# Kernel optimization log

Hardware: AMD Instinct MI355X
Metric: run time of the kernel (lower is better)

## Reference

```python
import jax, jax.numpy as jnp
import numpy as np

N, F_IN, H, P, R = 50000, 384, 128, 128, 16
E = 500000


def _lin_params(key, fan_in, fan_out):
    k1, k2 = jax.random.split(key)
    s = 1.0 / np.sqrt(fan_in)
    W = jax.random.uniform(k1, (fan_in, fan_out), jnp.float32, -s, s)
    b = jax.random.uniform(k2, (fan_out,), jnp.float32, -s, s)
    return W, b


def setup_inputs() -> dict:
    key = jax.random.key(0)
    ks = jax.random.split(key, 16)
    x = jax.random.normal(ks[0], (N, F_IN), jnp.float32)
    edge_index = jax.random.randint(ks[1], (2, E), 0, N, jnp.int64)
    W_gcn1, b_gcn1 = _lin_params(ks[2], F_IN, H)
    W_ti, b_ti = _lin_params(ks[3], F_IN, F_IN)      # CrossFusion.text_info (384 -> dim=384)
    W_gi, b_gi = _lin_params(ks[4], H, F_IN)          # CrossFusion.graph_info (128 -> 384)
    W_v, b_v = _lin_params(ks[5], F_IN, F_IN)         # CrossFusion.value
    Wl1, bl1 = _lin_params(ks[6], F_IN, F_IN // 2)    # left_generator hidden
    Wl2, bl2 = _lin_params(ks[7], F_IN // 2, P * R)
    Wr1, br1 = _lin_params(ks[8], F_IN, F_IN // 2)    # right_generator hidden
    Wr2, br2 = _lin_params(ks[9], F_IN // 2, R * F_IN)
    W_gcn2, b_gcn2 = _lin_params(ks[10], P, H)        # fusion_gcn (128 -> 128)
    W_gp, b_gp = _lin_params(ks[11], P, P)            # graph_proj
    return dict(x=x, edge_index=edge_index, W_gcn1=W_gcn1, b_gcn1=b_gcn1,
                W_ti=W_ti, b_ti=b_ti, W_gi=W_gi, b_gi=b_gi, W_v=W_v, b_v=b_v,
                Wl1=Wl1, bl1=bl1, Wl2=Wl2, bl2=bl2, Wr1=Wr1, br1=br1, Wr2=Wr2, br2=br2,
                W_gcn2=W_gcn2, b_gcn2=b_gcn2, W_gp=W_gp, b_gp=b_gp)


def _gcn(x, W, b, src, dst, n):
    # PyG GCNConv: self-loops + symmetric degree normalization, aggregate at dst.
    xw = x @ W
    loop = jnp.arange(n, dtype=src.dtype)
    s = jnp.concatenate([src, loop])
    d = jnp.concatenate([dst, loop])
    deg = jax.ops.segment_sum(jnp.ones_like(d, dtype=xw.dtype), d, num_segments=n)
    dinv = jnp.where(deg > 0, jax.lax.rsqrt(deg), 0.0)
    norm = dinv[s] * dinv[d]                           # [E+N]
    out = jax.ops.segment_sum(norm[:, None] * xw[s], d, num_segments=n)
    return out + b


def _cross_fusion(text_feat, graph_feat, row, col, W_ti, b_ti, W_gi, b_gi, W_v, b_v):
    n, dim = text_feat.shape[0], W_ti.shape[1]
    t_info = text_feat @ W_ti + b_ti                   # [N, dim]
    g_info = graph_feat @ W_gi + b_gi                  # [N, dim]
    v = text_feat @ W_v + b_v                          # [N, dim]
    scores = jnp.sum(t_info[row] * g_info[col], axis=-1) / np.sqrt(dim)   # [E]
    m = jax.ops.segment_max(scores, row, num_segments=n)                  # scatter_softmax
    e = jnp.exp(scores - m[row])
    denom = jax.ops.segment_sum(e, row, num_segments=n)
    attn = e / denom[row]
    out = jax.ops.segment_sum(attn[:, None] * v[col], row, num_segments=n)
    return out + text_feat


def _forward(x, edge_index, W_gcn1, b_gcn1, W_ti, b_ti, W_gi, b_gi, W_v, b_v,
             Wl1, bl1, Wl2, bl2, Wr1, br1, Wr2, br2, W_gcn2, b_gcn2, W_gp, b_gp):
    src, dst = edge_index[0], edge_index[1]
    n = x.shape[0]
    g_emb = _gcn(x, W_gcn1, b_gcn1, src, dst, n)
    x_fused = _cross_fusion(x, g_emb, src, dst, W_ti, b_ti, W_gi, b_gi, W_v, b_v)
    # N > 40000 -> low-rank chunked projection (chunking is pure batching; vectorize)
    left = (jax.nn.relu(x_fused @ Wl1 + bl1) @ Wl2 + bl2).reshape(n, P, R)
    right = (jax.nn.relu(x_fused @ Wr1 + br1) @ Wr2 + br2).reshape(n, R, F_IN)
    temp = jnp.einsum('nrf,nf->nr', right, x)
    p_t = jnp.einsum('npr,nr->np', left, temp)         # [N, P]
    g2 = _gcn(p_t, W_gcn2, b_gcn2, src, dst, n)        # dropout is identity in eval
    p_g = g2 @ W_gp + b_gp
    p_t = p_t / jnp.maximum(jnp.linalg.norm(p_t, axis=-1, keepdims=True), 1e-12)
    p_g = p_g / jnp.maximum(jnp.linalg.norm(p_g, axis=-1, keepdims=True), 1e-12)
    alignment = jnp.sum(p_t * p_g, axis=1)
    return alignment, p_t, p_g, g2


def reference(x, edge_index, W_gcn1, b_gcn1, W_ti, b_ti, W_gi, b_gi, W_v, b_v,
              Wl1, bl1, Wl2, bl2, Wr1, br1, Wr2, br2, W_gcn2, b_gcn2, W_gp, b_gp):
    return _forward(x, edge_index, W_gcn1, b_gcn1, W_ti, b_ti, W_gi, b_gi, W_v, b_v,
                    Wl1, bl1, Wl2, bl2, Wr1, br1, Wr2, br2, W_gcn2, b_gcn2, W_gp, b_gp)
```

## Files before the change

### kernel.cpp

```cpp
#include <hip/hip_runtime.h>

typedef unsigned int u32;
typedef unsigned short u16;
typedef short s16x8 __attribute__((ext_vector_type(8)));
typedef u16 u16x8 __attribute__((ext_vector_type(8)));
typedef float f32x4 __attribute__((ext_vector_type(4)));

#define FIN 384
#define HD  128
#define PD  128
#define RD  16

#define GLOAD16(g, l)                                                          \
  __builtin_amdgcn_global_load_lds(                                            \
      (const __attribute__((address_space(1))) void*)(g),                      \
      (__attribute__((address_space(3))) void*)(l), 16, 0, 0)

__device__ __forceinline__ u16 f2bf(float f) {
  u32 u = __float_as_uint(f);
  u32 r = (u + 0x7fffu + ((u >> 16) & 1u)) >> 16;
  return (u16)r;
}
__device__ __forceinline__ float bf2f(u16 h) {
  return __uint_as_float(((u32)h) << 16);
}

__device__ __forceinline__ int xcd_wgid() {
  int nwg = gridDim.x, orig = blockIdx.x;
  int q = nwg >> 3, r = nwg & 7, xcd = orig & 7, idx = orig >> 3;
  return (xcd < r ? xcd * (q + 1) : r * (q + 1) + (xcd - r) * q) + idx;
}

struct CvtEnt { const float* s; u16* d; int K, N, mode, blk0; };
struct CvtDesc { CvtEnt e[12]; int n; };

__global__ void cvt_all_k(CvtDesc dsc) {
  int b = blockIdx.x;
  int ei = 0;
  while (ei + 1 < dsc.n && dsc.e[ei + 1].blk0 <= b) ++ei;
  CvtEnt E = dsc.e[ei];
  int i = (b - E.blk0) * 256 + (int)threadIdx.x;
  int tot = E.K * E.N;
  if (i >= tot) return;
  float v;
  if (E.mode == 0) {
    int c = i / E.K, k = i - c * E.K;
    v = E.s[(size_t)k * E.N + c];
  } else if (E.mode == 1) {
    v = E.s[i];
  } else {
    int q = i / 384, f = i - q * 384;
    v = E.s[(size_t)(q >> 4) * 6144 + (q & 15) * 384 + f];
  }
  E.d[i] = f2bf(v);
}

__global__ void hist_k(const int* __restrict__ src, const int* __restrict__ dst,
                       u32* __restrict__ cnt, int n, int E) {
  int i = blockIdx.x * 256 + threadIdx.x;
  if (i < E) {
    atomicAdd(&cnt[src[i]], 1u);
    atomicAdd(&cnt[n + dst[i]], 1u);
  }
}

__global__ __launch_bounds__(1024)
void scanA_k(const u32* __restrict__ cnt, u32* __restrict__ off,
             u32* __restrict__ bsum, int n2) {
  __shared__ u32 sh[1024];
  int i = blockIdx.x * 1024 + (int)threadIdx.x;
  u32 v = (i < n2) ? cnt[i] : 0u;
  sh[threadIdx.x] = v;
  __syncthreads();
  for (int s = 1; s < 1024; s <<= 1) {
    u32 t = (threadIdx.x >= (u32)s) ? sh[threadIdx.x - s] : 0u;
    __syncthreads();
    sh[threadIdx.x] += t;
    __syncthreads();
  }
  if (i < n2) off[i] = sh[threadIdx.x] - v;
  if (threadIdx.x == 1023) bsum[blockIdx.x] = sh[1023];
}

__global__ void scanB_k(u32* __restrict__ bsum, int nb) {
  int l = threadIdx.x;
  u32 carry = 0u;
  for (int base = 0; base < nb; base += 64) {
    u32 v = (base + l < nb) ? bsum[base + l] : 0u;
    for (int s = 1; s < 64; s <<= 1) {
      u32 t = __shfl_up(v, s);
      if (l >= s) v += t;
    }
    if (base + l < nb) bsum[base + l] = v + carry;
    carry += __shfl(v, 63);
  }
}

__global__ __launch_bounds__(1024)
void scanC_k(u32* __restrict__ off, u32* __restrict__ cur,
             const u32* __restrict__ bsum, int n2) {
  int b = blockIdx.x;
  int i = b * 1024 + (int)threadIdx.x;
  if (i >= n2) return;
  u32 add = (b > 0) ? bsum[b - 1] : 0u;
  u32 o = off[i] + add;
  off[i] = o;
  cur[i] = o;
}

__global__ void fill_k(const int* __restrict__ src, const int* __restrict__ dst,
                       u32* __restrict__ cur, u32* __restrict__ adj, int n, int E) {
  int i = blockIdx.x * 256 + threadIdx.x;
  if (i >= E) return;
  int s = src[i], d = dst[i];
  u32 ps = atomicAdd(&cur[s], 1u);
  adj[ps] = (u32)d;
  u32 pd = atomicAdd(&cur[n + d], 1u);
  adj[pd] = (u32)s;
}

__global__ void dinv_k(const u32* __restrict__ cd, float* __restrict__ dinv, int n) {
  int i = blockIdx.x * 256 + threadIdx.x;
  if (i < n) dinv[i] = 1.0f / sqrtf((float)(cd[i] + 1u));
}

template <int WF32, int WBF>
__global__ void gcn_agg_k(const u16* __restrict__ xw, const float* __restrict__ dinv,
                          const u32* __restrict__ off, const u32* __restrict__ cnt,
                          const u32* __restrict__ nbr, const float* __restrict__ bias,
                          float* __restrict__ outf, u16* __restrict__ outb, int n) {
  int node = (blockIdx.x * blockDim.x + threadIdx.x) >> 6;
  int lane = threadIdx.x & 63;
  if (node >= n) return;
  float di = dinv[node];
  ushort2 v = ((const ushort2*)(xw + (size_t)node * HD))[lane];
  float ax = di * di * bf2f(v.x), ay = di * di * bf2f(v.y);
  u32 i = off[node], end = i + cnt[node];
  for (; i + 2 <= end; i += 2) {
    int s0 = (int)nbr[i], s1 = (int)nbr[i + 1];
    float w0 = di * dinv[s0], w1 = di * dinv[s1];
    ushort2 u0 = ((const ushort2*)(xw + (size_t)s0 * HD))[lane];
    ushort2 u1 = ((const ushort2*)(xw + (size_t)s1 * HD))[lane];
    ax = fmaf(w0, bf2f(u0.x), ax);
    ay = fmaf(w0, bf2f(u0.y), ay);
    ax = fmaf(w1, bf2f(u1.x), ax);
    ay = fmaf(w1, bf2f(u1.y), ay);
  }
  if (i < end) {
    int s0 = (int)nbr[i];
    float w0 = di * dinv[s0];
    ushort2 u0 = ((const ushort2*)(xw + (size_t)s0 * HD))[lane];
    ax = fmaf(w0, bf2f(u0.x), ax);
    ay = fmaf(w0, bf2f(u0.y), ay);
  }
  float2 b = ((const float2*)bias)[lane];
  ax += b.x; ay += b.y;
  if (WF32) ((float2*)(outf + (size_t)node * HD))[lane] = make_float2(ax, ay);
  if (WBF) {
    ushort2 ob; ob.x = f2bf(ax); ob.y = f2bf(ay);
    ((ushort2*)(outb + (size_t)node * HD))[lane] = ob;
  }
}

__global__ void attn_fused_k(const u32* __restrict__ off, const u32* __restrict__ cnt,
                             const u32* __restrict__ adj,
                             const u16* __restrict__ ti, int TS,
                             const u16* __restrict__ gi, int GS,
                             const u16* __restrict__ vmat, int VS,
                             const u16* __restrict__ xb,
                             float* __restrict__ scores,
                             u16* __restrict__ xf, int n) {
  int node = (blockIdx.x * blockDim.x + threadIdx.x) >> 6;
  int lane = threadIdx.x & 63;
  if (node >= n) return;
  u32 o = off[node], c = cnt[node];
  u32 end = o + c;
  float acc[6] = {0.f, 0.f, 0.f, 0.f, 0.f, 0.f};
  if (c > 0) {
    const u16* tp = ti + (size_t)node * TS;
    float tf[6];
#pragma unroll
    for (int q = 0; q < 3; ++q) {
      ushort2 tv = *(const ushort2*)(tp + q * 128 + lane * 2);
      tf[q * 2] = bf2f(tv.x);
      tf[q * 2 + 1] = bf2f(tv.y);
    }
    const float sc = 0.05103103630798288f;
    float mx = -1e30f;
    u32 i = o;
    for (; i + 2 <= end; i += 2) {
      int d0 = (int)adj[i], d1 = (int)adj[i + 1];
      const u16* g0 = gi + (size_t)d0 * GS;
      const u16* g1 = gi + (size_t)d1 * GS;
      float dot0 = 0.f, dot1 = 0.f;
#pragma unroll
      for (int q = 0; q < 3; ++q) {
        ushort2 a = *(const ushort2*)(g0 + q * 128 + lane * 2);
        ushort2 b = *(const ushort2*)(g1 + q * 128 + lane * 2);
        dot0 = fmaf(tf[q * 2], bf2f(a.x), dot0);
        dot0 = fmaf(tf[q * 2 + 1], bf2f(a.y), dot0);
        dot1 = fmaf(tf[q * 2], bf2f(b.x), dot1);
        dot1 = fmaf(tf[q * 2 + 1], bf2f(b.y), dot1);
      }
#pragma unroll
      for (int s2 = 32; s2 >= 1; s2 >>= 1) {
        dot0 += __shfl_xor(dot0, s2);
        dot1 += __shfl_xor(dot1, s2);
      }
      dot0 *= sc; dot1 *= sc;
      if (lane == 0) { scores[i] = dot0; scores[i + 1] = dot1; }
      mx = fmaxf(mx, fmaxf(dot0, dot1));
    }
    if (i < end) {
      int d0 = (int)adj[i];
      const u16* g0 = gi + (size_t)d0 * GS;
      float dot0 = 0.f;
#pragma unroll
      for (int q = 0; q < 3; ++q) {
        ushort2 a = *(const ushort2*)(g0 + q * 128 + lane * 2);
        dot0 = fmaf(tf[q * 2], bf2f(a.x), dot0);
        dot0 = fmaf(tf[q * 2 + 1], bf2f(a.y), dot0);
      }
#pragma unroll
      for (int s2 = 32; s2 >= 1; s2 >>= 1) dot0 += __shfl_xor(dot0, s2);
      dot0 *= sc;
      if (lane == 0) scores[i] = dot0;
      mx = fmaxf(mx, dot0);
    }
    float den = 0.f;
    for (u32 k = o + lane; k < end; k += 64) den += expf(scores[k] - mx);
#pragma unroll
    for (int s2 = 32; s2 >= 1; s2 >>= 1) den += __shfl_xor(den, s2);
    float invden = 1.0f / den;
    i = o;
    for (; i + 2 <= end; i += 2) {
      int d0 = (int)adj[i], d1 = (int)adj[i + 1];
      float w0 = expf(scores[i] - mx) * invden;
      float w1 = expf(scores[i + 1] - mx) * invden;
      const u16* v0 = vmat + (size_t)d0 * VS;
      const u16* v1 = vmat + (size_t)d1 * VS;
#pragma unroll
      for (int q = 0; q < 3; ++q) {
        ushort2 a = *(const ushort2*)(v0 + q * 128 + lane * 2);
        ushort2 b = *(const ushort2*)(v1 + q * 128 + lane * 2);
        acc[q * 2]     = fmaf(w0, bf2f(a.x), acc[q * 2]);
        acc[q * 2 + 1] = fmaf(w0, bf2f(a.y), acc[q * 2 + 1]);
        acc[q * 2]     = fmaf(w1, bf2f(b.x), acc[q * 2]);
        acc[q * 2 + 1] = fmaf(w1, bf2f(b.y), acc[q * 2 + 1]);
      }
    }
    if (i < end) {
      int d0 = (int)adj[i];
      float w0 = expf(scores[i] - mx) * invden;
      const u16* v0 = vmat + (size_t)d0 * VS;
#pragma unroll
      for (int q = 0; q < 3; ++q) {
        ushort2 a = *(const ushort2*)(v0 + q * 128 + lane * 2);
        acc[q * 2]     = fmaf(w0, bf2f(a.x), acc[q * 2]);
        acc[q * 2 + 1] = fmaf(w0, bf2f(a.y), acc[q * 2 + 1]);
      }
    }
  }
  const u16* xp = xb + (size_t)node * FIN;
  u16* op = xf + (size_t)node * FIN;
#pragma unroll
  for (int q = 0; q < 3; ++q) {
    ushort2 xv = *(const ushort2*)(xp + q * 128 + lane * 2);
    ushort2 ov;
    ov.x = f2bf(acc[q * 2] + bf2f(xv.x));
    ov.y = f2bf(acc[q * 2 + 1] + bf2f(xv.y));
    *(ushort2*)(op + q * 128 + lane * 2) = ov;
  }
}

template <int EPI, int OUTBF>
__global__ __launch_bounds__(256)
void mgemm_k(const u16* __restrict__ Abf, int As, const u16* __restrict__ WT,
             const float* __restrict__ bias, const float* __restrict__ bias_b, int bsplit,
             void* __restrict__ Cp, u16* __restrict__ Cbf2,
             float* __restrict__ tmp, int M, int K, int Nc, int ncx) {
  __shared__ u16 Albuf[2][128 * 32];
  __shared__ u16 Blbuf[2][128 * 32];
  const int t = threadIdx.x;
  const int lane = t & 63;
  const int wave = t >> 6;
  const int wr = wave >> 1, wc = wave & 1;
  const int wgid = xcd_wgid();
  const int ctile = wgid % ncx;
  const int row0 = (wgid / ncx) * 128;
  const int col0 = ctile * 128;
  const int sr = t >> 2;
  const int sk = (t & 3) * 8;
  const int nt = K >> 5;

  f32x4 acc[4][4] = {};

  auto stage = [&](int buf, int k0) {
#pragma unroll
    for (int h = 0; h < 2; ++h) {
      int ar = row0 + h * 64 + sr;
      if (ar >= M) ar = M - 1;
      GLOAD16(Abf + (size_t)ar * As + k0 + sk, &Albuf[buf][h * 2048 + wave * 512]);
    }
#pragma unroll
    for (int h = 0; h < 2; ++h) {
      int bc = col0 + h * 64 + sr;
      if (bc >= Nc) bc = Nc - 1;
      GLOAD16(WT + (size_t)bc * K + k0 + sk, &Blbuf[buf][h * 2048 + wave * 512]);
    }
  };

  stage(0, 0);
  int buf = 0;
  for (int tk = 0; tk < nt; ++tk) {
    __syncthreads();
    if (tk + 1 < nt) stage(buf ^ 1, (tk + 1) << 5);
    const u16* Al = Albuf[buf];
    const u16* Bl = Blbuf[buf];
    s16x8 a[4], b[4];
#pragma unroll
    for (int m = 0; m < 4; ++m)
      a[m] = *(const s16x8*)(Al + (wr * 64 + m * 16 + (lane & 15)) * 32 + (lane >> 4) * 8);
#pragma unroll
    for (int j = 0; j < 4; ++j)
      b[j] = *(const s16x8*)(Bl + (wc * 64 + j * 16 + (lane & 15)) * 32 + (lane >> 4) * 8);
#pragma unroll
    for (int m = 0; m < 4; ++m)
#pragma unroll
      for (int j = 0; j < 4; ++j)
        acc[m][j] = __builtin_amdgcn_mfma_f32_16x16x32_bf16(a[m], b[j], acc[m][j], 0, 0, 0);
    buf ^= 1;
  }

  if constexpr (EPI <= 2) {
#pragma unroll
    for (int m = 0; m < 4; ++m) {
      int rbase = row0 + wr * 64 + m * 16 + (lane >> 4) * 4;
#pragma unroll
      for (int j = 0; j < 4; ++j) {
        int col = col0 + wc * 64 + j * 16 + (lane & 15);
        if (col >= Nc) continue;
        float bv = 0.f;
        if (EPI >= 1) bv = (col < bsplit) ? bias[col] : bias_b[col - bsplit];
#pragma unroll
        for (int r = 0; r < 4; ++r) {
          int row = rbase + r;
          if (row >= M) continue;
          float v = acc[m][j][r] + bv;
          if (EPI == 2) v = fmaxf(v, 0.f);
          if (OUTBF) ((u16*)Cp)[(size_t)row * Nc + col] = f2bf(v);
          else       ((float*)Cp)[(size_t)row * Nc + col] = v;
        }
      }
    }
  } else if constexpr (EPI == 6) {
#pragma unroll
    for (int m = 0; m < 4; ++m) {
      int rbase = row0 + wr * 64 + m * 16 + (lane >> 4) * 4;
#pragma unroll
      for (int j = 0; j < 4; ++j) {
        int col = col0 + wc * 64 + j * 16 + (lane & 15);
        if (col < 2 * FIN) {
          float bv = (col < bsplit) ? bias[col] : bias_b[col - bsplit];
#pragma unroll
          for (int r = 0; r < 4; ++r) {
            int row = rbase + r;
            if (row >= M) continue;
            ((u16*)Cp)[(size_t)row * (2 * FIN) + col] = f2bf(acc[m][j][r] + bv);
          }
        } else {
          int c2 = col - 2 * FIN;
#pragma unroll
          for (int r = 0; r < 4; ++r) {
            int row = rbase + r;
            if (row >= M) continue;
            Cbf2[(size_t)row * HD + c2] = f2bf(acc[m][j][r]);
          }
        }
      }
    }
  } else {
    float* slice = (float*)Cp + (size_t)ctile * M * 8;
#pragma unroll
    for (int m = 0; m < 4; ++m) {
#pragma unroll
      for (int r = 0; r < 4; ++r) {
        int row = row0 + wr * 64 + m * 16 + (lane >> 4) * 4 + r;
        float tv = (row < M) ? tmp[(size_t)row * RD + (lane & 15)] : 0.f;
#pragma unroll
        for (int j = 0; j < 4; ++j) {
          float s = (acc[m][j][r] + bias[col0 + wc * 64 + j * 16 + (lane & 15)]) * tv;
          s += __shfl_xor(s, 1); s += __shfl_xor(s, 2);
          s += __shfl_xor(s, 4); s += __shfl_xor(s, 8);
          if ((lane & 15) == 0 && row < M)
            slice[(size_t)row * 8 + wc * 4 + j] = s;
        }
      }
    }
  }
}

__global__ void ptgather_k(const float* __restrict__ ptP, float* __restrict__ pt,
                           u16* __restrict__ ptb, int n) {
  int g = blockIdx.x * 256 + threadIdx.x;
  if (g >= n * 16) return;
  int row = g >> 4, ct = g & 15;
  const float* sp = ptP + ((size_t)ct * n + (size_t)row) * 8;
  float4 a = ((const float4*)sp)[0];
  float4 b = ((const float4*)sp)[1];
  float* dp = pt + (size_t)row * PD + ct * 8;
  ((float4*)dp)[0] = a;
  ((float4*)dp)[1] = b;
  ushort4 oa, ob;
  oa.x = f2bf(a.x); oa.y = f2bf(a.y); oa.z = f2bf(a.z); oa.w = f2bf(a.w);
  ob.x = f2bf(b.x); ob.y = f2bf(b.y); ob.z = f2bf(b.z); ob.w = f2bf(b.w);
  u16* db = ptb + (size_t)row * PD + ct * 8;
  ((ushort4*)db)[0] = oa;
  ((ushort4*)db)[1] = ob;
}

#define VM6  asm volatile("s_waitcnt vmcnt(6)" ::: "memory")
#define VM0  asm volatile("s_waitcnt vmcnt(0)" ::: "memory")
#define VMNOP
#define BARR asm volatile("s_barrier" ::: "memory")

__global__ __launch_bounds__(512)
void ygemm8_k(const u16* __restrict__ X, const u16* __restrict__ QT,
              const u16* __restrict__ Ar, float* __restrict__ tmpP, int M) {
  __shared__ u16 Al[2][16384];
  __shared__ u16 Bl[2][16384];
  const int t = threadIdx.x;
  const int lane = t & 63;
  const int wave = t >> 6;
  const int wr = wave >> 2;
  const int wcn = wave & 3;
  const int wgid = xcd_wgid();
  const int ctile = wgid % 12;
  const int row0 = (wgid / 12) * 256;
  const int col0 = ctile * 256;

  const int srow = t >> 3;
  const int sgk  = (((t & 7) ^ (srow & 7)) << 3);
  const int sdst = t * 8;

  const int pc0 = (((lane >> 4)) ^ (lane & 7)) << 3;
  const int pc1 = ((((lane >> 4) + 4)) ^ (lane & 7)) << 3;
  const int arow = (wr * 128 + (lane & 15)) << 6;
  const int brow = (wcn * 64 + (lane & 15)) << 6;

  f32x4 acc[8][4] = {};
  s16x8 a[4][2], b[4][2];

#define STGA8(bf, h, kt) do {                                                  \
    int r0_ = row0 + (h) * 128 + srow;                                         \
    int r1_ = r0_ + 64;                                                        \
    if (r0_ >= M) r0_ = M - 1;                                                 \
    if (r1_ >= M) r1_ = M - 1;                                                 \
    GLOAD16(X + (size_t)r0_ * 384 + (kt) * 64 + sgk, &Al[bf][(h) * 8192 + sdst]);        \
    GLOAD16(X + (size_t)r1_ * 384 + (kt) * 64 + sgk, &Al[bf][(h) * 8192 + 4096 + sdst]); \
  } while (0)

#define STGB8(bf, h, kt) do {                                                  \
    int c0_ = col0 + (h) * 128 + srow;                                         \
    GLOAD16(QT + (size_t)c0_ * 384 + (kt) * 64 + sgk, &Bl[bf][(h) * 8192 + sdst]);       \
    GLOAD16(QT + (size_t)(c0_ + 64) * 384 + (kt) * 64 + sgk,                   \
            &Bl[bf][(h) * 8192 + 4096 + sdst]);                                \
  } while (0)

#define LDA8(bf, mh) do {                                                      \
    _Pragma("unroll") for (int m2_ = 0; m2_ < 4; ++m2_) {                      \
      const u16* p_ = &Al[bf][arow + ((mh) * 4 + m2_) * 1024];                 \
      a[m2_][0] = *(const s16x8*)(p_ + pc0);                                   \
      a[m2_][1] = *(const s16x8*)(p_ + pc1);                                   \
    }                                                                          \
  } while (0)

#define LDB8(bf, jh) do {                                                      \
    _Pragma("unroll") for (int j2_ = 0; j2_ < 2; ++j2_) {                      \
      const u16* p_ = &Bl[bf][brow + ((jh) * 2 + j2_) * 1024];                 \
      b[(jh) * 2 + j2_][0] = *(const s16x8*)(p_ + pc0);                        \
      b[(jh) * 2 + j2_][1] = *(const s16x8*)(p_ + pc1);                        \
    }                                                                          \
  } while (0)

#define MQ8(mh, jh) do {                                                       \
    __builtin_amdgcn_s_setprio(1);                                             \
    _Pragma("unroll") for (int m2_ = 0; m2_ < 4; ++m2_)                        \
      _Pragma("unroll") for (int j2_ = 0; j2_ < 2; ++j2_)                      \
        _Pragma("unroll") for (int ks_ = 0; ks_ < 2; ++ks_)                    \
          acc[(mh) * 4 + m2_][(jh) * 2 + j2_] =                                \
              __builtin_amdgcn_mfma_f32_16x16x32_bf16(                         \
                  a[m2_][ks_], b[(jh) * 2 + j2_][ks_],                         \
                  acc[(mh) * 4 + m2_][(jh) * 2 + j2_], 0, 0, 0);               \
    __builtin_amdgcn_s_setprio(0);                                             \
  } while (0)

  STGA8(0, 0, 0); STGA8(0, 1, 0); STGB8(0, 0, 0); STGB8(0, 1, 0);
  STGA8(1, 0, 1); STGB8(1, 0, 1); STGB8(1, 1, 1);
  VM6; BARR;

#define ITER8(i, VMP3, VMP7, DOSTG)                                                          \
   LDA8(0,0); LDB8(0,0); STGA8(1,1,2*(i)+1);                   BARR; MQ8(0,0); BARR;  \
   LDB8(0,1);                                                  BARR; MQ8(0,1); BARR;  \
   LDA8(0,1); if (DOSTG) STGB8(0,0,2*(i)+2);                   BARR; MQ8(1,0); BARR;  \
   if (DOSTG) { STGB8(0,1,2*(i)+2); STGA8(0,0,2*(i)+2); } VMP3; BARR; MQ8(1,1); BARR; \
   LDA8(1,0); LDB8(1,0); if (DOSTG) STGA8(0,1,2*(i)+2);        BARR; MQ8(0,0); BARR;  \
   LDB8(1,1);                                                  BARR; MQ8(0,1); BARR;  \
   LDA8(1,1); if (DOSTG) STGB8(1,0,2*(i)+3);                   BARR; MQ8(1,0); BARR;  \
   if (DOSTG) { STGB8(1,1,2*(i)+3); STGA8(1,0,2*(i)+3); } VMP7; BARR; MQ8(1,1); BARR;

  ITER8(0, VM6, VM6, 1)
  ITER8(1, VM6, VM6, 1)
  ITER8(2, VM0, VMNOP, 0)

  const int h0 = (col0 >> 4) + wcn * 4;
  float s[8][4];
#pragma unroll
  for (int m = 0; m < 8; ++m) {
#pragma unroll
    for (int rr = 0; rr < 4; ++rr) {
      int row = row0 + wr * 128 + m * 16 + (lane >> 4) * 4 + rr;
      int rc = row < M ? row : M - 1;
      ushort4 arv = *(const ushort4*)(Ar + (size_t)rc * 384 + h0);
      s[m][rr] = bf2f(arv.x) * acc[m][0][rr] + bf2f(arv.y) * acc[m][1][rr] +
                 bf2f(arv.z) * acc[m][2][rr] + bf2f(arv.w) * acc[m][3][rr];
    }
  }

  __syncthreads();
  float* redA = (float*)&Al[0][0];
  float* redB = redA + 4096;
  const int r16 = lane & 15;
  const int rlb = wr * 128 + (lane >> 4) * 4;
  if (wcn & 1) {
    float* red = (wcn == 1) ? redA : redB;
#pragma unroll
    for (int m = 0; m < 8; ++m)
#pragma unroll
      for (int rr = 0; rr < 4; ++rr)
        red[(rlb + m * 16 + rr) * 16 + r16] = s[m][rr];
  }
  __syncthreads();
  if (!(wcn & 1)) {
    float* red = (wcn == 0) ? redA : redB;
#pragma unroll
    for (int m = 0; m < 8; ++m)
#pragma unroll
      for (int rr = 0; rr < 4; ++rr)
        s[m][rr] += red[(rlb + m * 16 + rr) * 16 + r16];
  }
  __syncthreads();
  if (wcn == 2) {
#pragma unroll
    for (int m = 0; m < 8; ++m)
#pragma unroll
      for (int rr = 0; rr < 4; ++rr)
        redA[(rlb + m * 16 + rr) * 16 + r16] = s[m][rr];
  }
  __syncthreads();
  if (wcn == 0) {
    float* slice = tmpP + (size_t)ctile * M * RD;
#pragma unroll
    for (int m = 0; m < 8; ++m)
#pragma unroll
      for (int rr = 0; rr < 4; ++rr) {
        int row = row0 + rlb + m * 16 + rr;
        if (row < M)
          slice[(size_t)row * RD + r16] =
              s[m][rr] + redA[(rlb + m * 16 + rr) * 16 + r16];
      }
  }
#undef STGA8
#undef STGB8
#undef LDA8
#undef LDB8
#undef MQ8
#undef ITER8
}

__global__ void combine_k(const float* __restrict__ tmpP, float* __restrict__ temp,
                          size_t sl, int tot4) {
  int i = blockIdx.x * 256 + threadIdx.x;
  if (i >= tot4) return;
  float4 s = ((const float4*)(tmpP + 12 * sl))[i];
#pragma unroll
  for (int c = 0; c < 12; ++c) {
    float4 p = ((const float4*)(tmpP + (size_t)c * sl))[i];
    s.x += p.x; s.y += p.y; s.z += p.z; s.w += p.w;
  }
  ((float4*)temp)[i] = s;
}

__global__ void final_k(float* __restrict__ out, int n) {
  int node = (blockIdx.x * blockDim.x + threadIdx.x) >> 6;
  int lane = threadIdx.x & 63;
  if (node >= n) return;
  float* pt = out + n + (size_t)node * PD;
  float* pg = out + n + (size_t)n * PD + (size_t)node * PD;
  float2 t = ((float2*)pt)[lane];
  float2 g = ((float2*)pg)[lane];
  float tt = t.x * t.x + t.y * t.y;
  float gg = g.x * g.x + g.y * g.y;
  float tg = t.x * g.x + t.y * g.y;
#pragma unroll
  for (int s = 32; s >= 1; s >>= 1) {
    tt += __shfl_xor(tt, s);
    gg += __shfl_xor(gg, s);
    tg += __shfl_xor(tg, s);
  }
  float invt = 1.0f / fmaxf(sqrtf(tt), 1e-12f);
  float invg = 1.0f / fmaxf(sqrtf(gg), 1e-12f);
  ((float2*)pt)[lane] = make_float2(t.x * invt, t.y * invt);
  ((float2*)pg)[lane] = make_float2(g.x * invg, g.y * invg);
  if (lane == 0) out[node] = tg * invt * invg;
}

struct MgArgs {
  const u16* A; int As; const u16* WT;
  const float* b; const float* b2; int bsplit;
  void* C; u16* C2; float* tmp;
  int M, K, Nc;
};
template <int EPI, int OUTBF>
static void mg(const MgArgs& a, hipStream_t s) {
  int ncx = (a.Nc + 127) / 128, nry = (a.M + 127) / 128;
  mgemm_k<EPI, OUTBF><<<dim3(ncx * nry), 256, 0, s>>>(
      a.A, a.As, a.WT, a.b, a.b2, a.bsplit, a.C, a.C2, a.tmp,
      a.M, a.K, a.Nc, ncx);
}

extern "C" void kernel_launch(void* const* d_in, const int* in_sizes, int n_in,
                              void* d_out, int out_size, void* d_ws, size_t ws_size,
                              hipStream_t stream) {
  const float* x      = (const float*)d_in[0];
  const int*   ei     = (const int*)d_in[1];
  const float* W_gcn1 = (const float*)d_in[2];
  const float* b_gcn1 = (const float*)d_in[3];
  const float* W_ti   = (const float*)d_in[4];
  const float* b_ti   = (const float*)d_in[5];
  const float* W_gi   = (const float*)d_in[6];
  const float* b_gi   = (const float*)d_in[7];
  const float* W_v    = (const float*)d_in[8];
  const float* b_v    = (const float*)d_in[9];
  const float* Wl1    = (const float*)d_in[10];
  const float* bl1    = (const float*)d_in[11];
  const float* Wl2    = (const float*)d_in[12];
  const float* bl2    = (const float*)d_in[13];
  const float* Wr1    = (const float*)d_in[14];
  const float* br1    = (const float*)d_in[15];
  const float* Wr2    = (const float*)d_in[16];
  const float* br2    = (const float*)d_in[17];
  const float* W_gcn2 = (const float*)d_in[18];
  const float* b_gcn2 = (const float*)d_in[19];
  const float* W_gp   = (const float*)d_in[20];
  const float* b_gp   = (const float*)d_in[21];

  const int n = in_sizes[0] / FIN;
  const int E = in_sizes[1] / 2;
  const int* src = ei;
  const int* dst = ei + E;

  char* wsp = (char*)d_ws;
  auto carve = [&](size_t bytes) -> void* {
    void* p = (void*)wsp;
    wsp += (bytes + 255) & ~(size_t)255;
    return p;
  };
  u32* cnt      = (u32*)carve((size_t)2 * n * 4);
  u32* off      = (u32*)carve((size_t)2 * n * 4);
  u32* cur      = (u32*)carve((size_t)2 * n * 4);
  u32* bsum     = (u32*)carve(512);
  u32* adj      = (u32*)carve((size_t)2 * E * 4);
  float* dinv   = (float*)carve((size_t)n * 4);
  float* scores = (float*)carve((size_t)E * 4);
  float* temp   = (float*)carve((size_t)n * RD * 4);

  u16* xbf    = (u16*)carve((size_t)n * FIN * 2);
  u16* tvbf   = (u16*)carve((size_t)n * 2 * FIN * 2);
  u16* bufHbf = (u16*)carve((size_t)n * HD * 2);
  u16* gembf  = (u16*)carve((size_t)n * HD * 2);
  u16* ptbf   = (u16*)carve((size_t)n * PD * 2);
  u16* g2bf   = (u16*)carve((size_t)n * HD * 2);

  u16* gibf   = (u16*)carve((size_t)n * FIN * 2);
  u16* xfbf   = (u16*)carve((size_t)n * FIN * 2);
  size_t tmpP_bytes = (size_t)13 * n * RD * 4;
  size_t overlay    = (size_t)2 * n * FIN * 2;
  carve(tmpP_bytes > overlay ? tmpP_bytes - overlay : 0);
  float* tmpP = (float*)gibf;
  float* ptP  = tmpP;

  u16* WtvT   = (u16*)carve((size_t)2 * FIN * FIN * 2);
  u16* WgcnT  = (u16*)carve((size_t)HD * FIN * 2);
  u16* WgiT   = (u16*)carve((size_t)FIN * HD * 2);
  u16* WlrT   = (u16*)carve((size_t)FIN * FIN * 2);
  u16* Wl2T   = (u16*)carve((size_t)2048 * 192 * 2);
  u16* QT     = (u16*)carve((size_t)3072 * FIN * 2);
  u16* BrT    = (u16*)carve((size_t)RD * FIN * 2);
  u16* Wgcn2T = (u16*)carve((size_t)HD * PD * 2);
  u16* WgpT   = (u16*)carve((size_t)PD * PD * 2);

  u16* lrbf = tvbf;

  float* out    = (float*)d_out;
  float* pt_raw = out + n;
  float* pg_raw = out + n + (size_t)n * PD;
  float* g2     = out + n + (size_t)2 * n * PD;

  CvtDesc dsc;
  int nent = 0, blk = 0;
  auto addent = [&](const float* s, u16* d, int K, int N, int mode) {
    dsc.e[nent] = {s, d, K, N, mode, blk};
    blk += (K * N + 255) / 256;
    ++nent;
  };
  addent(x,      xbf,    n * FIN, 1, 1);
  addent(W_ti,   WtvT,   FIN, FIN, 0);
  addent(W_v,    WtvT + (size_t)FIN * FIN, FIN, FIN, 0);
  addent(W_gcn1, WgcnT,  FIN, HD,  0);
  addent(W_gi,   WgiT,   HD,  FIN, 0);
  addent(Wl1,    WlrT,   FIN, 192, 0);
  addent(Wr1,    WlrT + (size_t)192 * FIN, FIN, 192, 0);
  addent(Wl2,    Wl2T,   192, 2048, 0);
  addent(Wr2,    QT,     FIN, 3072, 2);
  addent(br2,    BrT,    RD * FIN, 1, 1);
  addent(W_gcn2, Wgcn2T, PD, HD, 0);
  addent(W_gp,   WgpT,   PD, PD, 0);
  dsc.n = nent;
  cvt_all_k<<<blk, 256, 0, stream>>>(dsc);

  hipMemsetAsync(cnt, 0, (size_t)2 * n * 4, stream);
  hist_k<<<(E + 255) / 256, 256, 0, stream>>>(src, dst, cnt, n, E);
  int n2 = 2 * n;
  int nb = (n2 + 1023) / 1024;
  scanA_k<<<nb, 1024, 0, stream>>>(cnt, off, bsum, n2);
  scanB_k<<<1, 64, 0, stream>>>(bsum, nb);
  scanC_k<<<nb, 1024, 0, stream>>>(off, cur, bsum, n2);
  fill_k<<<(E + 255) / 256, 256, 0, stream>>>(src, dst, cur, adj, n, E);
  dinv_k<<<(n + 255) / 256, 256, 0, stream>>>(cnt + n, dinv, n);

  MgArgs a{};

  a = {xbf, FIN, WtvT, b_ti, b_v, FIN, tvbf, bufHbf, nullptr, n, FIN, 896};
  mg<6, 1>(a, stream);
  gcn_agg_k<0, 1><<<(n + 3) / 4, 256, 0, stream>>>(bufHbf, dinv, off + n, cnt + n, adj,
                                                   b_gcn1, nullptr, gembf, n);

  a = {gembf, HD, WgiT, b_gi, nullptr, 1 << 30, gibf, nullptr, nullptr, n, HD, FIN};
  mg<1, 1>(a, stream);
  attn_fused_k<<<(n + 3) / 4, 256, 0, stream>>>(off, cnt, adj, tvbf, 2 * FIN, gibf, FIN,
                                                tvbf + FIN, 2 * FIN, xbf, scores, xfbf, n);

  a = {xfbf, FIN, WlrT, bl1, br1, 192, lrbf, nullptr, nullptr, n, FIN, FIN};
  mg<2, 1>(a, stream);

  a = {xbf, FIN, BrT, nullptr, nullptr, 1 << 30, tmpP + (size_t)12 * n * RD, nullptr,
       nullptr, n, FIN, RD};
  mg<0, 0>(a, stream);
  ygemm8_k<<<dim3(12 * ((n + 255) / 256)), 512, 0, stream>>>(xbf, QT, lrbf + 192,
                                                             tmpP, n);
  combine_k<<<(n * RD / 4 + 255) / 256, 256, 0, stream>>>(tmpP, temp, (size_t)n * RD,
                                                          n * RD / 4);

  a = {lrbf, FIN, Wl2T, bl2, nullptr, 1 << 30, ptP, nullptr, temp, n, 192, PD * RD};
  mg<4, 0>(a, stream);
  ptgather_k<<<(n * 16 + 255) / 256, 256, 0, stream>>>(ptP, pt_raw, ptbf, n);

  a = {ptbf, PD, Wgcn2T, nullptr, nullptr, 1 << 30, bufHbf, nullptr, nullptr, n, PD, HD};
  mg<0, 1>(a, stream);
  gcn_agg_k<1, 1><<<(n + 3) / 4, 256, 0, stream>>>(bufHbf, dinv, off + n, cnt + n, adj,
                                                   b_gcn2, g2, g2bf, n);
  a = {g2bf, HD, WgpT, b_gp, nullptr, 1 << 30, pg_raw, nullptr, nullptr, n, HD, PD};
  mg<1, 0>(a, stream);

  final_k<<<(n + 3) / 4, 256, 0, stream>>>(out, n);
}
```

Baseline: 933.0 us.

## Unroll GCN gather, keep attention scores in registers, store partial p_t in bf16

The GCN aggregation loop is unrolled to four neighbours per iteration so more gather loads are in flight. Attention for nodes with at most 64 neighbours keeps scores and softmax weights in lane registers, using shuffles instead of the global scores round trip. The EPI==4 GEMM epilogue preloads its tmp values before the main loop and writes the partial p_t slices as bf16, halving that intermediate traffic. The bf16 partials lower the precision of the fp32 p_t output and add register pressure in the GEMM.

```diff
diff --git a/kernel.cpp b/kernel.cpp
--- a/kernel.cpp
+++ b/kernel.cpp
@@ -136,17 +136,21 @@
   ushort2 v = ((const ushort2*)(xw + (size_t)node * HD))[lane];
   float ax = di * di * bf2f(v.x), ay = di * di * bf2f(v.y);
   u32 i = off[node], end = i + cnt[node];
-  for (; i + 2 <= end; i += 2) {
-    int s0 = (int)nbr[i], s1 = (int)nbr[i + 1];
+  for (; i + 4 <= end; i += 4) {
+    int s0 = (int)nbr[i],     s1 = (int)nbr[i + 1];
+    int s2 = (int)nbr[i + 2], s3 = (int)nbr[i + 3];
     float w0 = di * dinv[s0], w1 = di * dinv[s1];
+    float w2 = di * dinv[s2], w3 = di * dinv[s3];
     ushort2 u0 = ((const ushort2*)(xw + (size_t)s0 * HD))[lane];
     ushort2 u1 = ((const ushort2*)(xw + (size_t)s1 * HD))[lane];
-    ax = fmaf(w0, bf2f(u0.x), ax);
-    ay = fmaf(w0, bf2f(u0.y), ay);
-    ax = fmaf(w1, bf2f(u1.x), ax);
-    ay = fmaf(w1, bf2f(u1.y), ay);
-  }
-  if (i < end) {
+    ushort2 u2 = ((const ushort2*)(xw + (size_t)s2 * HD))[lane];
+    ushort2 u3 = ((const ushort2*)(xw + (size_t)s3 * HD))[lane];
+    ax = fmaf(w0, bf2f(u0.x), ax); ay = fmaf(w0, bf2f(u0.y), ay);
+    ax = fmaf(w1, bf2f(u1.x), ax); ay = fmaf(w1, bf2f(u1.y), ay);
+    ax = fmaf(w2, bf2f(u2.x), ax); ay = fmaf(w2, bf2f(u2.y), ay);
+    ax = fmaf(w3, bf2f(u3.x), ax); ay = fmaf(w3, bf2f(u3.y), ay);
+  }
+  for (; i < end; ++i) {
     int s0 = (int)nbr[i];
     float w0 = di * dinv[s0];
     ushort2 u0 = ((const ushort2*)(xw + (size_t)s0 * HD))[lane];
@@ -176,6 +180,7 @@
   u32 o = off[node], c = cnt[node];
   u32 end = o + c;
   float acc[6] = {0.f, 0.f, 0.f, 0.f, 0.f, 0.f};
+  const float sc = 0.05103103630798288f;
   if (c > 0) {
     const u16* tp = ti + (size_t)node * TS;
     float tf[6];
@@ -185,79 +190,117 @@
       tf[q * 2] = bf2f(tv.x);
       tf[q * 2 + 1] = bf2f(tv.y);
     }
-    const float sc = 0.05103103630798288f;
-    float mx = -1e30f;
-    u32 i = o;
-    for (; i + 2 <= end; i += 2) {
-      int d0 = (int)adj[i], d1 = (int)adj[i + 1];
-      const u16* g0 = gi + (size_t)d0 * GS;
-      const u16* g1 = gi + (size_t)d1 * GS;
-      float dot0 = 0.f, dot1 = 0.f;
-#pragma unroll
-      for (int q = 0; q < 3; ++q) {
-        ushort2 a = *(const ushort2*)(g0 + q * 128 + lane * 2);
-        ushort2 b = *(const ushort2*)(g1 + q * 128 + lane * 2);
-        dot0 = fmaf(tf[q * 2], bf2f(a.x), dot0);
-        dot0 = fmaf(tf[q * 2 + 1], bf2f(a.y), dot0);
-        dot1 = fmaf(tf[q * 2], bf2f(b.x), dot1);
-        dot1 = fmaf(tf[q * 2 + 1], bf2f(b.y), dot1);
-      }
-#pragma unroll
-      for (int s2 = 32; s2 >= 1; s2 >>= 1) {
-        dot0 += __shfl_xor(dot0, s2);
-        dot1 += __shfl_xor(dot1, s2);
-      }
-      dot0 *= sc; dot1 *= sc;
-      if (lane == 0) { scores[i] = dot0; scores[i + 1] = dot1; }
-      mx = fmaxf(mx, fmaxf(dot0, dot1));
-    }
-    if (i < end) {
-      int d0 = (int)adj[i];
-      const u16* g0 = gi + (size_t)d0 * GS;
-      float dot0 = 0.f;
-#pragma unroll
-      for (int q = 0; q < 3; ++q) {
-        ushort2 a = *(const ushort2*)(g0 + q * 128 + lane * 2);
-        dot0 = fmaf(tf[q * 2], bf2f(a.x), dot0);
-        dot0 = fmaf(tf[q * 2 + 1], bf2f(a.y), dot0);
-      }
-#pragma unroll
-      for (int s2 = 32; s2 >= 1; s2 >>= 1) dot0 += __shfl_xor(dot0, s2);
-      dot0 *= sc;
-      if (lane == 0) scores[i] = dot0;
-      mx = fmaxf(mx, dot0);
-    }
-    float den = 0.f;
-    for (u32 k = o + lane; k < end; k += 64) den += expf(scores[k] - mx);
-#pragma unroll
-    for (int s2 = 32; s2 >= 1; s2 >>= 1) den += __shfl_xor(den, s2);
-    float invden = 1.0f / den;
-    i = o;
-    for (; i + 2 <= end; i += 2) {
-      int d0 = (int)adj[i], d1 = (int)adj[i + 1];
-      float w0 = expf(scores[i] - mx) * invden;
-      float w1 = expf(scores[i + 1] - mx) * invden;
-      const u16* v0 = vmat + (size_t)d0 * VS;
-      const u16* v1 = vmat + (size_t)d1 * VS;
-#pragma unroll
-      for (int q = 0; q < 3; ++q) {
-        ushort2 a = *(const ushort2*)(v0 + q * 128 + lane * 2);
-        ushort2 b = *(const ushort2*)(v1 + q * 128 + lane * 2);
-        acc[q * 2]     = fmaf(w0, bf2f(a.x), acc[q * 2]);
-        acc[q * 2 + 1] = fmaf(w0, bf2f(a.y), acc[q * 2 + 1]);
-        acc[q * 2]     = fmaf(w1, bf2f(b.x), acc[q * 2]);
-        acc[q * 2 + 1] = fmaf(w1, bf2f(b.y), acc[q * 2 + 1]);
-      }
-    }
-    if (i < end) {
-      int d0 = (int)adj[i];
-      float w0 = expf(scores[i] - mx) * invden;
-      const u16* v0 = vmat + (size_t)d0 * VS;
-#pragma unroll
-      for (int q = 0; q < 3; ++q) {
-        ushort2 a = *(const ushort2*)(v0 + q * 128 + lane * 2);
-        acc[q * 2]     = fmaf(w0, bf2f(a.x), acc[q * 2]);
-        acc[q * 2 + 1] = fmaf(w0, bf2f(a.y), acc[q * 2 + 1]);
+    if (c <= 64) {
+      float sreg = -1e30f;
+      u32 i = o;
+      for (; i + 2 <= end; i += 2) {
+        int d0 = (int)adj[i], d1 = (int)adj[i + 1];
+        const u16* g0 = gi + (size_t)d0 * GS;
+        const u16* g1 = gi + (size_t)d1 * GS;
+        float dot0 = 0.f, dot1 = 0.f;
+#pragma unroll
+        for (int q = 0; q < 3; ++q) {
+          ushort2 a = *(const ushort2*)(g0 + q * 128 + lane * 2);
+          ushort2 b = *(const ushort2*)(g1 + q * 128 + lane * 2);
+          dot0 = fmaf(tf[q * 2], bf2f(a.x), dot0);
+          dot0 = fmaf(tf[q * 2 + 1], bf2f(a.y), dot0);
+          dot1 = fmaf(tf[q * 2], bf2f(b.x), dot1);
+          dot1 = fmaf(tf[q * 2 + 1], bf2f(b.y), dot1);
+        }
+#pragma unroll
+        for (int s2 = 32; s2 >= 1; s2 >>= 1) {
+          dot0 += __shfl_xor(dot0, s2);
+          dot1 += __shfl_xor(dot1, s2);
+        }
+        int idx = (int)(i - o);
+        if (lane == idx) sreg = dot0 * sc;
+        if (lane == idx + 1) sreg = dot1 * sc;
+      }
+      if (i < end) {
+        int d0 = (int)adj[i];
+        const u16* g0 = gi + (size_t)d0 * GS;
+        float dot0 = 0.f;
+#pragma unroll
+        for (int q = 0; q < 3; ++q) {
+          ushort2 a = *(const ushort2*)(g0 + q * 128 + lane * 2);
+          dot0 = fmaf(tf[q * 2], bf2f(a.x), dot0);
+          dot0 = fmaf(tf[q * 2 + 1], bf2f(a.y), dot0);
+        }
+#pragma unroll
+        for (int s2 = 32; s2 >= 1; s2 >>= 1) dot0 += __shfl_xor(dot0, s2);
+        if (lane == (int)(i - o)) sreg = dot0 * sc;
+      }
+      float mx = sreg;
+#pragma unroll
+      for (int s2 = 32; s2 >= 1; s2 >>= 1) mx = fmaxf(mx, __shfl_xor(mx, s2));
+      float ew = (lane < (int)c) ? expf(sreg - mx) : 0.f;
+      float den = ew;
+#pragma unroll
+      for (int s2 = 32; s2 >= 1; s2 >>= 1) den += __shfl_xor(den, s2);
+      float wreg = ew / den;
+      i = o;
+      for (; i + 2 <= end; i += 2) {
+        int d0 = (int)adj[i], d1 = (int)adj[i + 1];
+        int idx = (int)(i - o);
+        float w0 = __shfl(wreg, idx);
+        float w1 = __shfl(wreg, idx + 1);
+        const u16* v0 = vmat + (size_t)d0 * VS;
+        const u16* v1 = vmat + (size_t)d1 * VS;
+#pragma unroll
+        for (int q = 0; q < 3; ++q) {
+          ushort2 a = *(const ushort2*)(v0 + q * 128 + lane * 2);
+          ushort2 b = *(const ushort2*)(v1 + q * 128 + lane * 2);
+          acc[q * 2]     = fmaf(w0, bf2f(a.x), acc[q * 2]);
+          acc[q * 2 + 1] = fmaf(w0, bf2f(a.y), acc[q * 2 + 1]);
+          acc[q * 2]     = fmaf(w1, bf2f(b.x), acc[q * 2]);
+          acc[q * 2 + 1] = fmaf(w1, bf2f(b.y), acc[q * 2 + 1]);
+        }
+      }
+      if (i < end) {
+        int d0 = (int)adj[i];
+        float w0 = __shfl(wreg, (int)(i - o));
+        const u16* v0 = vmat + (size_t)d0 * VS;
+#pragma unroll
+        for (int q = 0; q < 3; ++q) {
+          ushort2 a = *(const ushort2*)(v0 + q * 128 + lane * 2);
+          acc[q * 2]     = fmaf(w0, bf2f(a.x), acc[q * 2]);
+          acc[q * 2 + 1] = fmaf(w0, bf2f(a.y), acc[q * 2 + 1]);
+        }
+      }
+    } else {
+      float mx = -1e30f;
+      u32 i = o;
+      for (; i < end; ++i) {
+        int d0 = (int)adj[i];
+        const u16* g0 = gi + (size_t)d0 * GS;
+        float dot0 = 0.f;
+#pragma unroll
+        for (int q = 0; q < 3; ++q) {
+          ushort2 a = *(const ushort2*)(g0 + q * 128 + lane * 2);
+          dot0 = fmaf(tf[q * 2], bf2f(a.x), dot0);
+          dot0 = fmaf(tf[q * 2 + 1], bf2f(a.y), dot0);
+        }
+#pragma unroll
+        for (int s2 = 32; s2 >= 1; s2 >>= 1) dot0 += __shfl_xor(dot0, s2);
+        dot0 *= sc;
+        if (lane == 0) scores[i] = dot0;
+        mx = fmaxf(mx, dot0);
+      }
+      float den = 0.f;
+      for (u32 k = o + lane; k < end; k += 64) den += expf(scores[k] - mx);
+#pragma unroll
+      for (int s2 = 32; s2 >= 1; s2 >>= 1) den += __shfl_xor(den, s2);
+      float invden = 1.0f / den;
+      for (i = o; i < end; ++i) {
+        int d0 = (int)adj[i];
+        float w0 = expf(scores[i] - mx) * invden;
+        const u16* v0 = vmat + (size_t)d0 * VS;
+#pragma unroll
+        for (int q = 0; q < 3; ++q) {
+          ushort2 a = *(const ushort2*)(v0 + q * 128 + lane * 2);
+          acc[q * 2]     = fmaf(w0, bf2f(a.x), acc[q * 2]);
+          acc[q * 2 + 1] = fmaf(w0, bf2f(a.y), acc[q * 2 + 1]);
+        }
       }
     }
   }
@@ -295,6 +338,15 @@
 
   f32x4 acc[4][4] = {};
 
+  float tvp[16];
+  if constexpr (EPI == 4) {
+#pragma unroll
+    for (int mr = 0; mr < 16; ++mr) {
+      int row = row0 + wr * 64 + (mr >> 2) * 16 + (lane >> 4) * 4 + (mr & 3);
+      tvp[mr] = (row < M) ? tmp[(size_t)row * RD + (lane & 15)] : 0.f;
+    }
+  }
+
   auto stage = [&](int buf, int k0) {
 #pragma unroll
     for (int h = 0; h < 2; ++h) {
@@ -380,43 +432,40 @@
       }
     }
   } else {
-    float* slice = (float*)Cp + (size_t)ctile * M * 8;
+    u16* slice = (u16*)Cp + (size_t)ctile * M * 8;
 #pragma unroll
     for (int m = 0; m < 4; ++m) {
 #pragma unroll
       for (int r = 0; r < 4; ++r) {
         int row = row0 + wr * 64 + m * 16 + (lane >> 4) * 4 + r;
-        float tv = (row < M) ? tmp[(size_t)row * RD + (lane & 15)] : 0.f;
+        float tv = tvp[m * 4 + r];
 #pragma unroll
         for (int j = 0; j < 4; ++j) {
           float s = (acc[m][j][r] + bias[col0 + wc * 64 + j * 16 + (lane & 15)]) * tv;
           s += __shfl_xor(s, 1); s += __shfl_xor(s, 2);
           s += __shfl_xor(s, 4); s += __shfl_xor(s, 8);
           if ((lane & 15) == 0 && row < M)
-            slice[(size_t)row * 8 + wc * 4 + j] = s;
-        }
-      }
-    }
-  }
-}
-
-__global__ void ptgather_k(const float* __restrict__ ptP, float* __restrict__ pt,
+            slice[(size_t)row * 8 + wc * 4 + j] = f2bf(s);
+        }
+      }
+    }
+  }
+}
+
+__global__ void ptgather_k(const u16* __restrict__ ptP, float* __restrict__ pt,
                            u16* __restrict__ ptb, int n) {
   int g = blockIdx.x * 256 + threadIdx.x;
   if (g >= n * 16) return;
   int row = g >> 4, ct = g & 15;
-  const float* sp = ptP + ((size_t)ct * n + (size_t)row) * 8;
-  float4 a = ((const float4*)sp)[0];
-  float4 b = ((const float4*)sp)[1];
+  const u16* sp = ptP + ((size_t)ct * n + (size_t)row) * 8;
+  ushort4 a = ((const ushort4*)sp)[0];
+  ushort4 b = ((const ushort4*)sp)[1];
   float* dp = pt + (size_t)row * PD + ct * 8;
-  ((float4*)dp)[0] = a;
-  ((float4*)dp)[1] = b;
-  ushort4 oa, ob;
-  oa.x = f2bf(a.x); oa.y = f2bf(a.y); oa.z = f2bf(a.z); oa.w = f2bf(a.w);
-  ob.x = f2bf(b.x); ob.y = f2bf(b.y); ob.z = f2bf(b.z); ob.w = f2bf(b.w);
+  ((float4*)dp)[0] = make_float4(bf2f(a.x), bf2f(a.y), bf2f(a.z), bf2f(a.w));
+  ((float4*)dp)[1] = make_float4(bf2f(b.x), bf2f(b.y), bf2f(b.z), bf2f(b.w));
   u16* db = ptb + (size_t)row * PD + ct * 8;
-  ((ushort4*)db)[0] = oa;
-  ((ushort4*)db)[1] = ob;
+  ((ushort4*)db)[0] = a;
+  ((ushort4*)db)[1] = b;
 }
 
 #define VM6  asm volatile("s_waitcnt vmcnt(6)" ::: "memory")
@@ -688,7 +737,7 @@
   size_t overlay    = (size_t)2 * n * FIN * 2;
   carve(tmpP_bytes > overlay ? tmpP_bytes - overlay : 0);
   float* tmpP = (float*)gibf;
-  float* ptP  = tmpP;
+  u16* ptP    = (u16*)gibf;
 
   u16* WtvT   = (u16*)carve((size_t)2 * FIN * FIN * 2);
   u16* WgcnT  = (u16*)carve((size_t)HD * FIN * 2);
```

Measured after the change: 937.4 us. No clear change (+0.5%).
